# Performance work log

Measured on AMD Instinct MI355X. Metric: run time of the kernel, lower is better.

The kernel has to match this reference:

```python
import jax, jax.numpy as jnp
import numpy as np

B, T, S, I, H = 64, 64, 512, 512, 512

def setup_inputs() -> dict:
    key = jax.random.key(0)
    ks = jax.random.split(key, 9)
    sc = 0.02
    return {
        "input": jax.random.normal(ks[0], (B, T, I), jnp.float32),
        "h0": jax.random.normal(ks[1], (B, H), jnp.float32),
        "c0": jax.random.normal(ks[2], (B, H), jnp.float32),
        "ctx": jax.random.normal(ks[3], (S, B, H), jnp.float32),
        "W_ih": jax.random.normal(ks[4], (4 * H, I), jnp.float32) * sc,
        "b_ih": jax.random.normal(ks[5], (4 * H,), jnp.float32) * sc,
        "W_hh": jax.random.normal(ks[6], (4 * H, H), jnp.float32) * sc,
        "b_hh": jax.random.normal(ks[7], (4 * H,), jnp.float32) * sc,
        "W_out": jax.random.normal(ks[8], (H, 2 * H), jnp.float32) * sc,
    }

def reference(input, h0, c0, ctx, W_ih, b_ih, W_hh, b_hh, W_out):
    ctx_b = ctx.transpose(1, 0, 2)          # (B, S, H)
    x_tm = input.transpose(1, 0, 2)          # (T, B, I) time-major

    def step(carry, x):
        hx, cx = carry
        gates = x @ W_ih.T + b_ih + hx @ W_hh.T + b_hh   # (B, 4H)
        i, f, g, o = jnp.split(gates, 4, axis=1)          # chunk order: in, forget, cell, out
        ct = jax.nn.sigmoid(f) * cx + jax.nn.sigmoid(i) * jnp.tanh(g)
        ht = jax.nn.sigmoid(o) * jnp.tanh(ct)
        # dot attention over source positions
        scores = jnp.einsum('bsh,bh->bs', ctx_b, ht)      # (B, S)
        attn = jax.nn.softmax(scores, axis=1)
        wc = jnp.einsum('bs,bsh->bh', attn, ctx_b)        # (B, H)
        h_tilde = jnp.tanh(jnp.concatenate([wc, ht], axis=1) @ W_out.T)
        return (ht, ct), h_tilde

    (hT, cT), out = jax.lax.scan(step, (h0, c0), x_tm)    # out: (T, B, H)
    return out.transpose(1, 0, 2), hT, cT
```

## Files before the change

### kernel.cpp

```cpp
#include <hip/hip_runtime.h>
#include <hip/hip_bf16.h>

#define NB 64
#define NT_ 64
#define NS 512
#define NI 512
#define NH 512
#define G4 2048
#define H2 1024
#define BT (NB*NT_)
#define RBLK 64
#define CPB 8
#define XWB 512
#define TRB 4096
#define WOB 128
#define GRID_MEGA (RBLK + XWB + TRB + WOB)

typedef __attribute__((ext_vector_type(8))) short short8;
typedef __attribute__((ext_vector_type(4))) float f32x4;

__device__ __forceinline__ short f2bs(float f) {
    __hip_bfloat16 h = __float2bfloat16(f);
    return *reinterpret_cast<short*>(&h);
}
__device__ __forceinline__ float bs2f(short s) {
    unsigned int u = ((unsigned int)(unsigned short)s) << 16;
    union { unsigned int u; float f; } c; c.u = u; return c.f;
}
__device__ __forceinline__ short8 ld8b(const __hip_bfloat16* p) {
    return *reinterpret_cast<const short8*>(p);
}
__device__ __forceinline__ void ld8f2(const float* p, short8& hi, short8& lo) {
    float4 a = *reinterpret_cast<const float4*>(p);
    float4 b = *reinterpret_cast<const float4*>(p + 4);
    float v[8] = {a.x,a.y,a.z,a.w,b.x,b.y,b.z,b.w};
    #pragma unroll
    for (int i = 0; i < 8; i++) {
        short h = f2bs(v[i]);
        hi[i] = h;
        lo[i] = f2bs(v[i] - bs2f(h));
    }
}
__device__ __forceinline__ float fsigm(float x){ return 1.f/(1.f + __expf(-x)); }
__device__ __forceinline__ float ftanh(float x){ float e = __expf(2.f*x); return 1.f - 2.f/(e + 1.f); }

__global__ __launch_bounds__(256) void hseq0_init(const float* __restrict__ h0,
                                                  __hip_bfloat16* __restrict__ hs_h,
                                                  __hip_bfloat16* __restrict__ hs_l,
                                                  unsigned* __restrict__ sync) {
    int i = blockIdx.x*256 + threadIdx.x;
    if (i < 2048) sync[i] = 0u;
    if (i < NB*NH) {
        float x = h0[i];
        __hip_bfloat16 h = __float2bfloat16(x);
        hs_h[i] = h;
        hs_l[i] = __float2bfloat16(x - __bfloat162float(h));
    }
}

__global__ __launch_bounds__(256, 1) void lstm_mega(
    const float* __restrict__ c0,
    const float* __restrict__ W_hh,
    const float* __restrict__ input,
    const float* __restrict__ W_ih,
    const float* __restrict__ b_ih,
    const float* __restrict__ b_hh,
    float* __restrict__ XW2,
    __hip_bfloat16* __restrict__ hs_h,
    __hip_bfloat16* __restrict__ hs_l,
    float* __restrict__ hT, float* __restrict__ cT,
    unsigned* __restrict__ flags,
    unsigned* __restrict__ xwcnt,
    const float* __restrict__ ctx,
    __hip_bfloat16* __restrict__ ctxT,
    const float* __restrict__ W_out,
    __hip_bfloat16* __restrict__ Wout_h,
    __hip_bfloat16* __restrict__ Wout_l)
{
    __shared__ __align__(16) char smem_raw[82432];
    int bid = blockIdx.x;
    int tid = threadIdx.x;
    int lane = tid & 63, w = tid >> 6;
    int fr = lane & 15, fq = lane >> 4;

    if (bid < RBLK) {
        __hip_bfloat16* Wh = (__hip_bfloat16*)smem_raw;
        __hip_bfloat16* Wl = (__hip_bfloat16*)(smem_raw + 32768);
        float (*gl)[32][33] = (float(*)[32][33])(smem_raw + 65536);
        int bi = bid;

        {
            int jl = tid >> 3, ck8 = tid & 7;
            int grow = (jl >> 3) * NH + bi * CPB + (jl & 7);
            const float* src = W_hh + (size_t)grow * NH;
            #pragma unroll
            for (int cc = 0; cc < 8; cc++) {
                int ck = ck8 * 8 + cc;
                short8 hi, lo;
                ld8f2(src + ck*8, hi, lo);
                int sw = (ck * 16) ^ ((jl & 7) << 4);
                *(short8*)((char*)Wh + jl * 1024 + sw) = hi;
                *(short8*)((char*)Wl + jl * 1024 + sw) = lo;
            }
        }
        int eb  = tid >> 2;
        int ec0 = (tid & 3) * 2;
        int ebl = eb & 31, mhalf = eb >> 5;
        float creg[2];
        creg[0] = c0[eb * NH + bi*CPB + ec0];
        creg[1] = c0[eb * NH + bi*CPB + ec0 + 1];
        {
            int guard = 0;
            while (__hip_atomic_load(&xwcnt[0], __ATOMIC_RELAXED, __HIP_MEMORY_SCOPE_AGENT) < 8u) {
                __builtin_amdgcn_s_sleep(1);
                if (++guard > (1<<22)) break;
            }
        }
        float xw[8];
        #pragma unroll
        for (int g = 0; g < 4; g++)
          #pragma unroll
          for (int u = 0; u < 2; u++)
            xw[g*2+u] = XW2[(size_t)eb*G4 + g*NH + bi*CPB + ec0 + u];
        __syncthreads();

        int m0 = (w & 1) * 32;
        int kbase = (w >> 1) * 256;

        for (int t = 0; t < NT_; t++) {
            const __hip_bfloat16* Ah = hs_h + (size_t)t * NB * NH;
            const __hip_bfloat16* Al = hs_l + (size_t)t * NB * NH;

            short8 Aregh[2][8], Aregl[2][8];
            #pragma unroll
            for (int i = 0; i < 2; i++) {
                const __hip_bfloat16* rowH = Ah + (size_t)(m0 + i*16 + fr) * NH + kbase + fq*8;
                const __hip_bfloat16* rowL = Al + (size_t)(m0 + i*16 + fr) * NH + kbase + fq*8;
                #pragma unroll
                for (int k8 = 0; k8 < 8; k8++) {
                    Aregh[i][k8] = ld8b(rowH + k8*32);
                    Aregl[i][k8] = ld8b(rowL + k8*32);
                }
            }

            f32x4 acc[2][2] = {};
            #pragma unroll
            for (int k8 = 0; k8 < 8; k8++) {
                short8 b_h[2], b_l[2];
                #pragma unroll
                for (int j = 0; j < 2; j++) {
                    int jl = j*16 + fr;
                    int byt = jl*1024 + ((((kbase + k8*32 + fq*8)*2)) ^ ((jl & 7) << 4));
                    b_h[j] = *(const short8*)((const char*)Wh + byt);
                    b_l[j] = *(const short8*)((const char*)Wl + byt);
                }
                #pragma unroll
                for (int i = 0; i < 2; i++)
                    #pragma unroll
                    for (int j = 0; j < 2; j++) {
                        acc[i][j] = __builtin_amdgcn_mfma_f32_16x16x32_bf16(Aregh[i][k8], b_h[j], acc[i][j], 0,0,0);
                        acc[i][j] = __builtin_amdgcn_mfma_f32_16x16x32_bf16(Aregh[i][k8], b_l[j], acc[i][j], 0,0,0);
                        acc[i][j] = __builtin_amdgcn_mfma_f32_16x16x32_bf16(Aregl[i][k8], b_h[j], acc[i][j], 0,0,0);
                    }
            }
            #pragma unroll
            for (int i = 0; i < 2; i++)
              #pragma unroll
              for (int j = 0; j < 2; j++)
                #pragma unroll
                for (int r = 0; r < 4; r++)
                    gl[w][i*16 + fq*4 + r][j*16 + fr] = acc[i][j][r];
            __syncthreads();

            float hv[2];
            #pragma unroll
            for (int u = 0; u < 2; u++) {
                int cl = ec0 + u;
                float gi = gl[mhalf][ebl][cl]      + gl[2+mhalf][ebl][cl]      + xw[u];
                float gf = gl[mhalf][ebl][8 + cl]  + gl[2+mhalf][ebl][8 + cl]  + xw[2+u];
                float gg = gl[mhalf][ebl][16 + cl] + gl[2+mhalf][ebl][16 + cl] + xw[4+u];
                float go = gl[mhalf][ebl][24 + cl] + gl[2+mhalf][ebl][24 + cl] + xw[6+u];
                float ct = fsigm(gf)*creg[u] + fsigm(gi)*ftanh(gg);
                hv[u] = fsigm(go)*ftanh(ct);
                creg[u] = ct;
            }
            int hcol = bi*CPB + ec0;
            size_t hoff = (size_t)(t+1)*NB*NH + (size_t)eb*NH + hcol;
            unsigned short h0b = (unsigned short)f2bs(hv[0]);
            unsigned short h1b = (unsigned short)f2bs(hv[1]);
            unsigned ph = (unsigned)h0b | ((unsigned)h1b << 16);
            unsigned short l0b = (unsigned short)f2bs(hv[0] - bs2f((short)h0b));
            unsigned short l1b = (unsigned short)f2bs(hv[1] - bs2f((short)h1b));
            unsigned pl = (unsigned)l0b | ((unsigned)l1b << 16);
            __hip_atomic_store((unsigned*)&hs_h[hoff], ph, __ATOMIC_RELAXED, __HIP_MEMORY_SCOPE_AGENT);
            __hip_atomic_store((unsigned*)&hs_l[hoff], pl, __ATOMIC_RELAXED, __HIP_MEMORY_SCOPE_AGENT);
            if (t == NT_-1) {
                *(float2*)&hT[(size_t)eb*NH + hcol] = make_float2(hv[0], hv[1]);
                *(float2*)&cT[(size_t)eb*NH + hcol] = make_float2(creg[0], creg[1]);
            }

            asm volatile("s_waitcnt vmcnt(0)" ::: "memory");
            __syncthreads();
            if (tid == 0)
                __hip_atomic_store(&flags[bi*16], (unsigned)(t+1), __ATOMIC_RELAXED, __HIP_MEMORY_SCOPE_AGENT);
            if (t + 1 < NT_) {
                int guard = 0;
                while (__hip_atomic_load(&xwcnt[(t+1)*16], __ATOMIC_RELAXED, __HIP_MEMORY_SCOPE_AGENT) < 8u) {
                    __builtin_amdgcn_s_sleep(1);
                    if (++guard > (1<<22)) break;
                }
                #pragma unroll
                for (int g = 0; g < 4; g++)
                  #pragma unroll
                  for (int u = 0; u < 2; u++)
                    xw[g*2+u] = XW2[((size_t)(t+1)*NB + eb)*G4 + g*NH + bi*CPB + ec0 + u];
            }
            {
                unsigned target = (unsigned)(t+1);
                int guard = 0;
                while (__hip_atomic_load(&flags[lane*16], __ATOMIC_RELAXED, __HIP_MEMORY_SCOPE_AGENT) < target) {
                    __builtin_amdgcn_s_sleep(1);
                    if (++guard > (1<<22)) break;
                }
            }
        }
    } else if (bid < RBLK + XWB) {
        int e  = bid - RBLK;
        int t0 = e >> 3;
        int n0 = ((e & 7) * 4 + w) * 64;
        f32x4 acc[4][4] = {};
        for (int kk = 0; kk < NI; kk += 32) {
            short8 ah[4], al[4], bh[4], bl[4];
            #pragma unroll
            for (int i = 0; i < 4; i++)
                ld8f2(input + ((size_t)(i*16+fr)*NT_ + t0)*NI + kk + fq*8, ah[i], al[i]);
            #pragma unroll
            for (int j = 0; j < 4; j++)
                ld8f2(W_ih + (size_t)(n0+j*16+fr)*NI + kk + fq*8, bh[j], bl[j]);
            #pragma unroll
            for (int i = 0; i < 4; i++)
                #pragma unroll
                for (int j = 0; j < 4; j++) {
                    acc[i][j] = __builtin_amdgcn_mfma_f32_16x16x32_bf16(ah[i], bh[j], acc[i][j], 0,0,0);
                    acc[i][j] = __builtin_amdgcn_mfma_f32_16x16x32_bf16(ah[i], bl[j], acc[i][j], 0,0,0);
                    acc[i][j] = __builtin_amdgcn_mfma_f32_16x16x32_bf16(al[i], bh[j], acc[i][j], 0,0,0);
                }
        }
        #pragma unroll
        for (int i = 0; i < 4; i++)
          #pragma unroll
          for (int j = 0; j < 4; j++)
            #pragma unroll
            for (int r = 0; r < 4; r++) {
                int b = i*16 + fq*4 + r;
                int n = n0 + j*16 + fr;
                float v = acc[i][j][r] + b_ih[n] + b_hh[n];
                union { float f; unsigned u; } cv; cv.f = v;
                __hip_atomic_store((unsigned*)&XW2[((size_t)t0*NB + b)*G4 + n], cv.u,
                                   __ATOMIC_RELAXED, __HIP_MEMORY_SCOPE_AGENT);
            }
        asm volatile("s_waitcnt vmcnt(0)" ::: "memory");
        __syncthreads();
        if (tid == 0)
            __hip_atomic_fetch_add(&xwcnt[t0*16], 1u, __ATOMIC_RELAXED, __HIP_MEMORY_SCOPE_AGENT);
    } else if (bid < RBLK + XWB + TRB) {
        float (*tile)[65] = (float(*)[65])smem_raw;
        int tr = bid - (RBLK + XWB);
        int s0 = (tr & 7) * 64, h0 = ((tr >> 3) & 7) * 64, b = tr >> 6;
        int tx = tid & 63, ty = tid >> 6;
        for (int i = 0; i < 16; i++) {
            int s = i*4 + ty;
            tile[s][tx] = ctx[(size_t)(s0+s)*NB*NH + (size_t)b*NH + h0 + tx];
        }
        __syncthreads();
        for (int i = 0; i < 16; i++) {
            int h = i*4 + ty;
            ctxT[(size_t)b*NH*NS + (size_t)(h0+h)*NS + s0 + tx] = __float2bfloat16(tile[tx][h]);
        }
    } else {
        int wv = bid - (RBLK + XWB + TRB);
        for (int i = wv*256 + tid; i < NH*H2; i += WOB*256) {
            float x = W_out[i];
            __hip_bfloat16 h = __float2bfloat16(x);
            Wout_h[i] = h;
            Wout_l[i] = __float2bfloat16(x - __bfloat162float(h));
        }
    }
}

__global__ __launch_bounds__(256) void gemm_scores(const __hip_bfloat16* __restrict__ hs_h,
                                                   const __hip_bfloat16* __restrict__ hs_l,
                                                   const float* __restrict__ ctx,
                                                   float* __restrict__ scores) {
    int wid = blockIdx.x*4 + (threadIdx.x>>6);
    int lane = threadIdx.x & 63;
    int b  = wid >> 3;
    int n0 = (wid & 7) * 64;
    int fr = lane & 15, fq = lane >> 4;
    const __hip_bfloat16* Abh = hs_h + NB*NH + (size_t)b*NH;
    const __hip_bfloat16* Abl = hs_l + NB*NH + (size_t)b*NH;
    const float* Bb = ctx + (size_t)b*NH;
    f32x4 acc[4][4] = {};
    for (int kk = 0; kk < NH; kk += 32) {
        short8 ah[4], al[4], bh[4], bl[4];
        #pragma unroll
        for (int i = 0; i < 4; i++) {
            size_t off = (size_t)(i*16+fr)*NB*NH + kk + fq*8;
            ah[i] = ld8b(Abh + off);
            al[i] = ld8b(Abl + off);
        }
        #pragma unroll
        for (int j = 0; j < 4; j++) ld8f2(Bb + (size_t)(n0+j*16+fr)*NB*NH + kk + fq*8, bh[j], bl[j]);
        #pragma unroll
        for (int i = 0; i < 4; i++)
            #pragma unroll
            for (int j = 0; j < 4; j++) {
                acc[i][j] = __builtin_amdgcn_mfma_f32_16x16x32_bf16(ah[i], bh[j], acc[i][j], 0,0,0);
                acc[i][j] = __builtin_amdgcn_mfma_f32_16x16x32_bf16(ah[i], bl[j], acc[i][j], 0,0,0);
                acc[i][j] = __builtin_amdgcn_mfma_f32_16x16x32_bf16(al[i], bh[j], acc[i][j], 0,0,0);
            }
    }
    #pragma unroll
    for (int i = 0; i < 4; i++)
      #pragma unroll
      for (int j = 0; j < 4; j++)
        #pragma unroll
        for (int r = 0; r < 4; r++) {
            int t = i*16 + fq*4 + r;
            int s = n0 + j*16 + fr;
            scores[((size_t)b*NT_ + t)*NS + s] = acc[i][j][r];
        }
}

__global__ __launch_bounds__(256) void softmax_rows(const float* __restrict__ scores,
                                                    __hip_bfloat16* __restrict__ ah,
                                                    __hip_bfloat16* __restrict__ al) {
    int row = blockIdx.x*4 + (threadIdx.x>>6);
    int lane = threadIdx.x & 63;
    const float* r = scores + (size_t)row*NS;
    float v[8], mx = -1e30f;
    #pragma unroll
    for (int i = 0; i < 8; i++) { v[i] = r[lane + i*64]; mx = fmaxf(mx, v[i]); }
    #pragma unroll
    for (int off = 32; off; off >>= 1) mx = fmaxf(mx, __shfl_xor(mx, off));
    float sum = 0.f;
    #pragma unroll
    for (int i = 0; i < 8; i++) { v[i] = __expf(v[i]-mx); sum += v[i]; }
    #pragma unroll
    for (int off = 32; off; off >>= 1) sum += __shfl_xor(sum, off);
    float inv = 1.f/sum;
    #pragma unroll
    for (int i = 0; i < 8; i++) {
        float a = v[i]*inv;
        __hip_bfloat16 h = __float2bfloat16(a);
        ah[(size_t)row*NS + lane + i*64] = h;
        al[(size_t)row*NS + lane + i*64] = __float2bfloat16(a - __bfloat162float(h));
    }
}

__global__ __launch_bounds__(256) void gemm_wc(const __hip_bfloat16* __restrict__ Ah,
                                               const __hip_bfloat16* __restrict__ Al,
                                               const __hip_bfloat16* __restrict__ ctxT,
                                               float* __restrict__ Wc) {
    int wid = blockIdx.x*4 + (threadIdx.x>>6);
    int lane = threadIdx.x & 63;
    int b  = wid >> 3;
    int n0 = (wid & 7) * 64;
    int fr = lane & 15, fq = lane >> 4;
    const __hip_bfloat16* Abh = Ah + (size_t)b*NT_*NS;
    const __hip_bfloat16* Abl = Al + (size_t)b*NT_*NS;
    const __hip_bfloat16* Bb  = ctxT + (size_t)b*NH*NS;
    f32x4 acc[4][4] = {};
    for (int kk = 0; kk < NS; kk += 32) {
        short8 ah[4], al[4], bb[4];
        #pragma unroll
        for (int i = 0; i < 4; i++) {
            ah[i] = ld8b(Abh + (size_t)(i*16+fr)*NS + kk + fq*8);
            al[i] = ld8b(Abl + (size_t)(i*16+fr)*NS + kk + fq*8);
        }
        #pragma unroll
        for (int j = 0; j < 4; j++) bb[j] = ld8b(Bb + (size_t)(n0+j*16+fr)*NS + kk + fq*8);
        #pragma unroll
        for (int i = 0; i < 4; i++)
            #pragma unroll
            for (int j = 0; j < 4; j++) {
                acc[i][j] = __builtin_amdgcn_mfma_f32_16x16x32_bf16(ah[i], bb[j], acc[i][j], 0,0,0);
                acc[i][j] = __builtin_amdgcn_mfma_f32_16x16x32_bf16(al[i], bb[j], acc[i][j], 0,0,0);
            }
    }
    #pragma unroll
    for (int i = 0; i < 4; i++)
      #pragma unroll
      for (int j = 0; j < 4; j++)
        #pragma unroll
        for (int r = 0; r < 4; r++) {
            int t = i*16 + fq*4 + r;
            int h = n0 + j*16 + fr;
            Wc[((size_t)b*NT_ + t)*NH + h] = acc[i][j][r];
        }
}

__global__ __launch_bounds__(256) void gemm_out(const float* __restrict__ Wc,
                                                const __hip_bfloat16* __restrict__ hs_h,
                                                const __hip_bfloat16* __restrict__ hs_l,
                                                const __hip_bfloat16* __restrict__ Wh,
                                                const __hip_bfloat16* __restrict__ Wl,
                                                float* __restrict__ out) {
    int wid = blockIdx.x*4 + (threadIdx.x>>6);
    int lane = threadIdx.x & 63;
    int m0 = (wid >> 3) * 64;
    int n0 = (wid & 7) * 64;
    int fr = lane & 15, fq = lane >> 4;
    f32x4 acc[4][4] = {};
    for (int kk = 0; kk < NH; kk += 32) {
        short8 ah[4], al[4], bh[4], bl[4];
        #pragma unroll
        for (int i = 0; i < 4; i++) ld8f2(Wc + (size_t)(m0+i*16+fr)*NH + kk + fq*8, ah[i], al[i]);
        #pragma unroll
        for (int j = 0; j < 4; j++) {
            bh[j] = ld8b(Wh + (size_t)(n0+j*16+fr)*H2 + kk + fq*8);
            bl[j] = ld8b(Wl + (size_t)(n0+j*16+fr)*H2 + kk + fq*8);
        }
        #pragma unroll
        for (int i = 0; i < 4; i++)
            #pragma unroll
            for (int j = 0; j < 4; j++) {
                acc[i][j] = __builtin_amdgcn_mfma_f32_16x16x32_bf16(ah[i], bh[j], acc[i][j], 0,0,0);
                acc[i][j] = __builtin_amdgcn_mfma_f32_16x16x32_bf16(ah[i], bl[j], acc[i][j], 0,0,0);
                acc[i][j] = __builtin_amdgcn_mfma_f32_16x16x32_bf16(al[i], bh[j], acc[i][j], 0,0,0);
            }
    }
    {
        const __hip_bfloat16* A2h = hs_h + NB*NH + (size_t)(m0>>6)*NH;
        const __hip_bfloat16* A2l = hs_l + NB*NH + (size_t)(m0>>6)*NH;
        for (int kk = 0; kk < NH; kk += 32) {
            short8 ah[4], al[4], bh[4], bl[4];
            #pragma unroll
            for (int i = 0; i < 4; i++) {
                size_t off = (size_t)(i*16+fr)*NB*NH + kk + fq*8;
                ah[i] = ld8b(A2h + off);
                al[i] = ld8b(A2l + off);
            }
            #pragma unroll
            for (int j = 0; j < 4; j++) {
                bh[j] = ld8b(Wh + (size_t)(n0+j*16+fr)*H2 + NH + kk + fq*8);
                bl[j] = ld8b(Wl + (size_t)(n0+j*16+fr)*H2 + NH + kk + fq*8);
            }
            #pragma unroll
            for (int i = 0; i < 4; i++)
                #pragma unroll
                for (int j = 0; j < 4; j++) {
                    acc[i][j] = __builtin_amdgcn_mfma_f32_16x16x32_bf16(ah[i], bh[j], acc[i][j], 0,0,0);
                    acc[i][j] = __builtin_amdgcn_mfma_f32_16x16x32_bf16(ah[i], bl[j], acc[i][j], 0,0,0);
                    acc[i][j] = __builtin_amdgcn_mfma_f32_16x16x32_bf16(al[i], bh[j], acc[i][j], 0,0,0);
                }
        }
    }
    #pragma unroll
    for (int i = 0; i < 4; i++)
      #pragma unroll
      for (int j = 0; j < 4; j++)
        #pragma unroll
        for (int r = 0; r < 4; r++) {
            int m = m0 + i*16 + fq*4 + r;
            int n = n0 + j*16 + fr;
            out[(size_t)m*NH + n] = ftanh(acc[i][j][r]);
        }
}


extern "C" void kernel_launch(void* const* d_in, const int* in_sizes, int n_in,
                              void* d_out, int out_size, void* d_ws, size_t ws_size,
                              hipStream_t stream) {
    const float* input = (const float*)d_in[0];
    const float* h0    = (const float*)d_in[1];
    const float* c0    = (const float*)d_in[2];
    const float* ctx   = (const float*)d_in[3];
    const float* W_ih  = (const float*)d_in[4];
    const float* b_ih  = (const float*)d_in[5];
    const float* W_hh  = (const float*)d_in[6];
    const float* b_hh  = (const float*)d_in[7];
    const float* W_out = (const float*)d_in[8];
    float* out = (float*)d_out;

    const size_t OFF_XW     = 0;
    const size_t OFF_SCORES = 0;
    const size_t OFF_ATTN_H = 8388608;
    const size_t OFF_ATTN_L = 12582912;
    const size_t OFF_HS_H   = 33554432;
    const size_t OFF_HS_L   = 37814272;
    const size_t OFF_SYNC   = 42074112;
    const size_t OFF_WC     = 42082304;
    const size_t OFF_WOUT_H = 58859520;
    const size_t OFF_WOUT_L = 59908096;
    const size_t OFF_CTXT   = 60956672;
    if (ws_size < 94511104u) return;

    char* ws = (char*)d_ws;
    float*          XW2    = (float*)(ws + OFF_XW);
    float*          scores = (float*)(ws + OFF_SCORES);
    __hip_bfloat16* attn_h = (__hip_bfloat16*)(ws + OFF_ATTN_H);
    __hip_bfloat16* attn_l = (__hip_bfloat16*)(ws + OFF_ATTN_L);
    __hip_bfloat16* hs_h   = (__hip_bfloat16*)(ws + OFF_HS_H);
    __hip_bfloat16* hs_l   = (__hip_bfloat16*)(ws + OFF_HS_L);
    unsigned*       sync   = (unsigned*)(ws + OFF_SYNC);
    unsigned*       flags  = sync;
    unsigned*       xwcnt  = sync + 1024;
    float*          Wc     = (float*)(ws + OFF_WC);
    __hip_bfloat16* Wout_h = (__hip_bfloat16*)(ws + OFF_WOUT_H);
    __hip_bfloat16* Wout_l = (__hip_bfloat16*)(ws + OFF_WOUT_L);
    __hip_bfloat16* ctxT   = (__hip_bfloat16*)(ws + OFF_CTXT);

    hseq0_init<<<128, 256, 0, stream>>>(h0, hs_h, hs_l, sync);

    float* hT = out + (size_t)BT*NH;
    float* cT = hT + NB*NH;
    lstm_mega<<<GRID_MEGA, 256, 0, stream>>>(c0, W_hh, input, W_ih,
                                             b_ih, b_hh, XW2, hs_h, hs_l, hT, cT,
                                             flags, xwcnt, ctx, ctxT, W_out, Wout_h, Wout_l);

    gemm_scores<<<128, 256, 0, stream>>>(hs_h, hs_l, ctx, scores);
    softmax_rows<<<1024, 256, 0, stream>>>(scores, attn_h, attn_l);
    gemm_wc<<<128, 256, 0, stream>>>(attn_h, attn_l, ctxT, Wc);
    gemm_out<<<128, 256, 0, stream>>>(Wc, hs_h, hs_l, Wout_h, Wout_l, out);
}
```

Measured before the change: 627.6 us.

## Fuse attention and output projection into mega kernel, overlapped with recurrence

Removes the four post-recurrence kernels (scores, softmax, weighted context, output GEMM) and adds 128 attention blocks to the persistent mega kernel. Each block handles one batch row and half the timesteps, spin-waiting on recurrence step flags so it can process 16-step chunks while the LSTM is still running. Transpose and W_out conversion blocks now publish completion counters so the attention blocks know when their inputs are ready. This aims to hide attention work behind the serial recurrence and drop the scores, attention and Wc round trips through global memory. In exchange it adds spin-wait polling and co-residency assumptions, and each block reloads ctx and W_out from global memory.

Result: slower. 673.8 us (+7.4%).

```diff
diff --git a/kernel.cpp b/kernel.cpp
--- a/kernel.cpp
+++ b/kernel.cpp
@@ -14,7 +14,8 @@
 #define XWB 512
 #define TRB 4096
 #define WOB 128
-#define GRID_MEGA (RBLK + XWB + TRB + WOB)
+#define ATT 128
+#define GRID_MEGA (RBLK + XWB + TRB + WOB + ATT)
 
 typedef __attribute__((ext_vector_type(8))) short short8;
 typedef __attribute__((ext_vector_type(4))) float f32x4;
@@ -49,7 +50,7 @@
                                                   __hip_bfloat16* __restrict__ hs_l,
                                                   unsigned* __restrict__ sync) {
     int i = blockIdx.x*256 + threadIdx.x;
-    if (i < 2048) sync[i] = 0u;
+    if (i < 4096) sync[i] = 0u;
     if (i < NB*NH) {
         float x = h0[i];
         __hip_bfloat16 h = __float2bfloat16(x);
@@ -71,11 +72,14 @@
     float* __restrict__ hT, float* __restrict__ cT,
     unsigned* __restrict__ flags,
     unsigned* __restrict__ xwcnt,
+    unsigned* __restrict__ trcnt,
+    unsigned* __restrict__ wocnt,
     const float* __restrict__ ctx,
     __hip_bfloat16* __restrict__ ctxT,
     const float* __restrict__ W_out,
     __hip_bfloat16* __restrict__ Wout_h,
-    __hip_bfloat16* __restrict__ Wout_l)
+    __hip_bfloat16* __restrict__ Wout_l,
+    float* __restrict__ out)
 {
     __shared__ __align__(16) char smem_raw[82432];
     int bid = blockIdx.x;
@@ -88,7 +92,6 @@
         __hip_bfloat16* Wl = (__hip_bfloat16*)(smem_raw + 32768);
         float (*gl)[32][33] = (float(*)[32][33])(smem_raw + 65536);
         int bi = bid;
-
         {
             int jl = tid >> 3, ck8 = tid & 7;
             int grow = (jl >> 3) * NH + bi * CPB + (jl & 7);
@@ -130,7 +133,6 @@
         for (int t = 0; t < NT_; t++) {
             const __hip_bfloat16* Ah = hs_h + (size_t)t * NB * NH;
             const __hip_bfloat16* Al = hs_l + (size_t)t * NB * NH;
-
             short8 Aregh[2][8], Aregl[2][8];
             #pragma unroll
             for (int i = 0; i < 2; i++) {
@@ -142,7 +144,6 @@
                     Aregl[i][k8] = ld8b(rowL + k8*32);
                 }
             }
-
             f32x4 acc[2][2] = {};
             #pragma unroll
             for (int k8 = 0; k8 < 8; k8++) {
@@ -198,7 +199,6 @@
                 *(float2*)&hT[(size_t)eb*NH + hcol] = make_float2(hv[0], hv[1]);
                 *(float2*)&cT[(size_t)eb*NH + hcol] = make_float2(creg[0], creg[1]);
             }
-
             asm volatile("s_waitcnt vmcnt(0)" ::: "memory");
             __syncthreads();
             if (tid == 0)
@@ -273,199 +273,183 @@
             tile[s][tx] = ctx[(size_t)(s0+s)*NB*NH + (size_t)b*NH + h0 + tx];
         }
         __syncthreads();
-        for (int i = 0; i < 16; i++) {
-            int h = i*4 + ty;
-            ctxT[(size_t)b*NH*NS + (size_t)(h0+h)*NS + s0 + tx] = __float2bfloat16(tile[tx][h]);
-        }
+        for (int i = 0; i < 8; i++) {
+            int h = i*8 + (tid >> 5);
+            int cp = tid & 31;
+            unsigned short v0 = (unsigned short)f2bs(tile[2*cp][h]);
+            unsigned short v1 = (unsigned short)f2bs(tile[2*cp+1][h]);
+            unsigned pv = (unsigned)v0 | ((unsigned)v1 << 16);
+            __hip_atomic_store((unsigned*)&ctxT[(size_t)b*NH*NS + (size_t)(h0+h)*NS + s0 + 2*cp],
+                               pv, __ATOMIC_RELAXED, __HIP_MEMORY_SCOPE_AGENT);
+        }
+        asm volatile("s_waitcnt vmcnt(0)" ::: "memory");
+        __syncthreads();
+        if (tid == 0)
+            __hip_atomic_fetch_add(&trcnt[b*16], 1u, __ATOMIC_RELAXED, __HIP_MEMORY_SCOPE_AGENT);
+    } else if (bid < RBLK + XWB + TRB + WOB) {
+        int wv = bid - (RBLK + XWB + TRB);
+        for (int p = wv*256 + tid; p < NH*H2/2; p += WOB*256) {
+            float x0 = W_out[2*p], x1 = W_out[2*p+1];
+            unsigned short h0b = (unsigned short)f2bs(x0);
+            unsigned short h1b = (unsigned short)f2bs(x1);
+            unsigned short l0b = (unsigned short)f2bs(x0 - bs2f((short)h0b));
+            unsigned short l1b = (unsigned short)f2bs(x1 - bs2f((short)h1b));
+            __hip_atomic_store((unsigned*)Wout_h + p, (unsigned)h0b | ((unsigned)h1b << 16),
+                               __ATOMIC_RELAXED, __HIP_MEMORY_SCOPE_AGENT);
+            __hip_atomic_store((unsigned*)Wout_l + p, (unsigned)l0b | ((unsigned)l1b << 16),
+                               __ATOMIC_RELAXED, __HIP_MEMORY_SCOPE_AGENT);
+        }
+        asm volatile("s_waitcnt vmcnt(0)" ::: "memory");
+        __syncthreads();
+        if (tid == 0)
+            __hip_atomic_fetch_add(&wocnt[0], 1u, __ATOMIC_RELAXED, __HIP_MEMORY_SCOPE_AGENT);
     } else {
-        int wv = bid - (RBLK + XWB + TRB);
-        for (int i = wv*256 + tid; i < NH*H2; i += WOB*256) {
-            float x = W_out[i];
-            __hip_bfloat16 h = __float2bfloat16(x);
-            Wout_h[i] = h;
-            Wout_l[i] = __float2bfloat16(x - __bfloat162float(h));
+        int at = bid - (RBLK + XWB + TRB + WOB);
+        int b = at >> 1;
+        int halfsel = at & 1;
+        float (*S)[520] = (float(*)[520])smem_raw;
+        __hip_bfloat16 (*WcH)[520] = (__hip_bfloat16(*)[520])smem_raw;
+        __hip_bfloat16 (*WcL)[520] = (__hip_bfloat16(*)[520])(smem_raw + 16640);
+        __hip_bfloat16 (*AtH)[520] = (__hip_bfloat16(*)[520])(smem_raw + 33280);
+        __hip_bfloat16 (*AtL)[520] = (__hip_bfloat16(*)[520])(smem_raw + 49920);
+
+        {
+            int guard = 0;
+            while (__hip_atomic_load(&wocnt[0], __ATOMIC_RELAXED, __HIP_MEMORY_SCOPE_AGENT) < (unsigned)WOB) {
+                __builtin_amdgcn_s_sleep(1);
+                if (++guard > (1<<24)) break;
+            }
+            guard = 0;
+            while (__hip_atomic_load(&trcnt[b*16], __ATOMIC_RELAXED, __HIP_MEMORY_SCOPE_AGENT) < 64u) {
+                __builtin_amdgcn_s_sleep(1);
+                if (++guard > (1<<24)) break;
+            }
+        }
+
+        for (int tg = halfsel*2; tg < halfsel*2 + 2; tg++) {
+            int t0 = tg * 16;
+            {
+                unsigned target = (unsigned)(t0 + 16);
+                int guard = 0;
+                while (__hip_atomic_load(&flags[lane*16], __ATOMIC_RELAXED, __HIP_MEMORY_SCOPE_AGENT) < target) {
+                    __builtin_amdgcn_s_sleep(1);
+                    if (++guard > (1<<24)) break;
+                }
+            }
+
+            {
+                f32x4 sacc[8] = {};
+                const __hip_bfloat16* Ab = hs_h + (size_t)(t0+fr+1)*NB*NH + (size_t)b*NH;
+                const __hip_bfloat16* Al2 = hs_l + (size_t)(t0+fr+1)*NB*NH + (size_t)b*NH;
+                for (int kk = 0; kk < NH; kk += 32) {
+                    short8 ah = ld8b(Ab + kk + fq*8);
+                    short8 al = ld8b(Al2 + kk + fq*8);
+                    #pragma unroll
+                    for (int j = 0; j < 8; j++) {
+                        short8 bh, bl;
+                        ld8f2(ctx + (size_t)(w*128 + j*16 + fr)*NB*NH + (size_t)b*NH + kk + fq*8, bh, bl);
+                        sacc[j] = __builtin_amdgcn_mfma_f32_16x16x32_bf16(ah, bh, sacc[j], 0,0,0);
+                        sacc[j] = __builtin_amdgcn_mfma_f32_16x16x32_bf16(ah, bl, sacc[j], 0,0,0);
+                        sacc[j] = __builtin_amdgcn_mfma_f32_16x16x32_bf16(al, bh, sacc[j], 0,0,0);
+                    }
+                }
+                #pragma unroll
+                for (int j = 0; j < 8; j++)
+                  #pragma unroll
+                  for (int r = 0; r < 4; r++)
+                    S[fq*4 + r][w*128 + j*16 + fr] = sacc[j][r];
+            }
+            __syncthreads();
+
+            for (int rr = 0; rr < 4; rr++) {
+                int row = w*4 + rr;
+                float v[8], mx = -1e30f;
+                #pragma unroll
+                for (int i = 0; i < 8; i++) { v[i] = S[row][lane + i*64]; mx = fmaxf(mx, v[i]); }
+                #pragma unroll
+                for (int off = 32; off; off >>= 1) mx = fmaxf(mx, __shfl_xor(mx, off));
+                float sum = 0.f;
+                #pragma unroll
+                for (int i = 0; i < 8; i++) { v[i] = __expf(v[i]-mx); sum += v[i]; }
+                #pragma unroll
+                for (int off = 32; off; off >>= 1) sum += __shfl_xor(sum, off);
+                float inv = 1.f/sum;
+                #pragma unroll
+                for (int i = 0; i < 8; i++) {
+                    float a = v[i]*inv;
+                    short hb = f2bs(a);
+                    AtH[row][lane + i*64] = *(__hip_bfloat16*)&hb;
+                    short lb = f2bs(a - bs2f(hb));
+                    AtL[row][lane + i*64] = *(__hip_bfloat16*)&lb;
+                }
+            }
+            __syncthreads();
+
+            {
+                f32x4 wacc[8] = {};
+                const __hip_bfloat16* Bb = ctxT + (size_t)b*NH*NS;
+                for (int kk = 0; kk < NS; kk += 32) {
+                    short8 pah = *(const short8*)&AtH[fr][kk + fq*8];
+                    short8 pal = *(const short8*)&AtL[fr][kk + fq*8];
+                    #pragma unroll
+                    for (int j = 0; j < 8; j++) {
+                        short8 cb = ld8b(Bb + (size_t)(w*128 + j*16 + fr)*NS + kk + fq*8);
+                        wacc[j] = __builtin_amdgcn_mfma_f32_16x16x32_bf16(pah, cb, wacc[j], 0,0,0);
+                        wacc[j] = __builtin_amdgcn_mfma_f32_16x16x32_bf16(pal, cb, wacc[j], 0,0,0);
+                    }
+                }
+                #pragma unroll
+                for (int j = 0; j < 8; j++)
+                  #pragma unroll
+                  for (int r = 0; r < 4; r++) {
+                    float v = wacc[j][r];
+                    short hb = f2bs(v);
+                    WcH[fq*4 + r][w*128 + j*16 + fr] = *(__hip_bfloat16*)&hb;
+                    short lb = f2bs(v - bs2f(hb));
+                    WcL[fq*4 + r][w*128 + j*16 + fr] = *(__hip_bfloat16*)&lb;
+                  }
+            }
+            __syncthreads();
+
+            {
+                f32x4 oacc[8] = {};
+                for (int kk = 0; kk < NH; kk += 32) {
+                    short8 ah = *(const short8*)&WcH[fr][kk + fq*8];
+                    short8 al = *(const short8*)&WcL[fr][kk + fq*8];
+                    #pragma unroll
+                    for (int j = 0; j < 8; j++) {
+                        size_t wrow = (size_t)(w*128 + j*16 + fr)*H2 + kk + fq*8;
+                        short8 bh = ld8b(Wout_h + wrow);
+                        short8 bl = ld8b(Wout_l + wrow);
+                        oacc[j] = __builtin_amdgcn_mfma_f32_16x16x32_bf16(ah, bh, oacc[j], 0,0,0);
+                        oacc[j] = __builtin_amdgcn_mfma_f32_16x16x32_bf16(ah, bl, oacc[j], 0,0,0);
+                        oacc[j] = __builtin_amdgcn_mfma_f32_16x16x32_bf16(al, bh, oacc[j], 0,0,0);
+                    }
+                }
+                const __hip_bfloat16* A2h = hs_h + (size_t)(t0+fr+1)*NB*NH + (size_t)b*NH;
+                const __hip_bfloat16* A2l = hs_l + (size_t)(t0+fr+1)*NB*NH + (size_t)b*NH;
+                for (int kk = 0; kk < NH; kk += 32) {
+                    short8 ah = ld8b(A2h + kk + fq*8);
+                    short8 al = ld8b(A2l + kk + fq*8);
+                    #pragma unroll
+                    for (int j = 0; j < 8; j++) {
+                        size_t wrow = (size_t)(w*128 + j*16 + fr)*H2 + NH + kk + fq*8;
+                        short8 bh = ld8b(Wout_h + wrow);
+                        short8 bl = ld8b(Wout_l + wrow);
+                        oacc[j] = __builtin_amdgcn_mfma_f32_16x16x32_bf16(ah, bh, oacc[j], 0,0,0);
+                        oacc[j] = __builtin_amdgcn_mfma_f32_16x16x32_bf16(ah, bl, oacc[j], 0,0,0);
+                        oacc[j] = __builtin_amdgcn_mfma_f32_16x16x32_bf16(al, bh, oacc[j], 0,0,0);
+                    }
+                }
+                #pragma unroll
+                for (int j = 0; j < 8; j++)
+                  #pragma unroll
+                  for (int r = 0; r < 4; r++)
+                    out[(size_t)(b*64 + t0 + fq*4 + r)*NH + w*128 + j*16 + fr] = ftanh(oacc[j][r]);
+            }
+            __syncthreads();
         }
     }
-}
-
-__global__ __launch_bounds__(256) void gemm_scores(const __hip_bfloat16* __restrict__ hs_h,
-                                                   const __hip_bfloat16* __restrict__ hs_l,
-                                                   const float* __restrict__ ctx,
-                                                   float* __restrict__ scores) {
-    int wid = blockIdx.x*4 + (threadIdx.x>>6);
-    int lane = threadIdx.x & 63;
-    int b  = wid >> 3;
-    int n0 = (wid & 7) * 64;
-    int fr = lane & 15, fq = lane >> 4;
-    const __hip_bfloat16* Abh = hs_h + NB*NH + (size_t)b*NH;
-    const __hip_bfloat16* Abl = hs_l + NB*NH + (size_t)b*NH;
-    const float* Bb = ctx + (size_t)b*NH;
-    f32x4 acc[4][4] = {};
-    for (int kk = 0; kk < NH; kk += 32) {
-        short8 ah[4], al[4], bh[4], bl[4];
-        #pragma unroll
-        for (int i = 0; i < 4; i++) {
-            size_t off = (size_t)(i*16+fr)*NB*NH + kk + fq*8;
-            ah[i] = ld8b(Abh + off);
-            al[i] = ld8b(Abl + off);
-        }
-        #pragma unroll
-        for (int j = 0; j < 4; j++) ld8f2(Bb + (size_t)(n0+j*16+fr)*NB*NH + kk + fq*8, bh[j], bl[j]);
-        #pragma unroll
-        for (int i = 0; i < 4; i++)
-            #pragma unroll
-            for (int j = 0; j < 4; j++) {
-                acc[i][j] = __builtin_amdgcn_mfma_f32_16x16x32_bf16(ah[i], bh[j], acc[i][j], 0,0,0);
-                acc[i][j] = __builtin_amdgcn_mfma_f32_16x16x32_bf16(ah[i], bl[j], acc[i][j], 0,0,0);
-                acc[i][j] = __builtin_amdgcn_mfma_f32_16x16x32_bf16(al[i], bh[j], acc[i][j], 0,0,0);
-            }
-    }
-    #pragma unroll
-    for (int i = 0; i < 4; i++)
-      #pragma unroll
-      for (int j = 0; j < 4; j++)
-        #pragma unroll
-        for (int r = 0; r < 4; r++) {
-            int t = i*16 + fq*4 + r;
-            int s = n0 + j*16 + fr;
-            scores[((size_t)b*NT_ + t)*NS + s] = acc[i][j][r];
-        }
-}
-
-__global__ __launch_bounds__(256) void softmax_rows(const float* __restrict__ scores,
-                                                    __hip_bfloat16* __restrict__ ah,
-                                                    __hip_bfloat16* __restrict__ al) {
-    int row = blockIdx.x*4 + (threadIdx.x>>6);
-    int lane = threadIdx.x & 63;
-    const float* r = scores + (size_t)row*NS;
-    float v[8], mx = -1e30f;
-    #pragma unroll
-    for (int i = 0; i < 8; i++) { v[i] = r[lane + i*64]; mx = fmaxf(mx, v[i]); }
-    #pragma unroll
-    for (int off = 32; off; off >>= 1) mx = fmaxf(mx, __shfl_xor(mx, off));
-    float sum = 0.f;
-    #pragma unroll
-    for (int i = 0; i < 8; i++) { v[i] = __expf(v[i]-mx); sum += v[i]; }
-    #pragma unroll
-    for (int off = 32; off; off >>= 1) sum += __shfl_xor(sum, off);
-    float inv = 1.f/sum;
-    #pragma unroll
-    for (int i = 0; i < 8; i++) {
-        float a = v[i]*inv;
-        __hip_bfloat16 h = __float2bfloat16(a);
-        ah[(size_t)row*NS + lane + i*64] = h;
-        al[(size_t)row*NS + lane + i*64] = __float2bfloat16(a - __bfloat162float(h));
-    }
-}
-
-__global__ __launch_bounds__(256) void gemm_wc(const __hip_bfloat16* __restrict__ Ah,
-                                               const __hip_bfloat16* __restrict__ Al,
-                                               const __hip_bfloat16* __restrict__ ctxT,
-                                               float* __restrict__ Wc) {
-    int wid = blockIdx.x*4 + (threadIdx.x>>6);
-    int lane = threadIdx.x & 63;
-    int b  = wid >> 3;
-    int n0 = (wid & 7) * 64;
-    int fr = lane & 15, fq = lane >> 4;
-    const __hip_bfloat16* Abh = Ah + (size_t)b*NT_*NS;
-    const __hip_bfloat16* Abl = Al + (size_t)b*NT_*NS;
-    const __hip_bfloat16* Bb  = ctxT + (size_t)b*NH*NS;
-    f32x4 acc[4][4] = {};
-    for (int kk = 0; kk < NS; kk += 32) {
-        short8 ah[4], al[4], bb[4];
-        #pragma unroll
-        for (int i = 0; i < 4; i++) {
-            ah[i] = ld8b(Abh + (size_t)(i*16+fr)*NS + kk + fq*8);
-            al[i] = ld8b(Abl + (size_t)(i*16+fr)*NS + kk + fq*8);
-        }
-        #pragma unroll
-        for (int j = 0; j < 4; j++) bb[j] = ld8b(Bb + (size_t)(n0+j*16+fr)*NS + kk + fq*8);
-        #pragma unroll
-        for (int i = 0; i < 4; i++)
-            #pragma unroll
-            for (int j = 0; j < 4; j++) {
-                acc[i][j] = __builtin_amdgcn_mfma_f32_16x16x32_bf16(ah[i], bb[j], acc[i][j], 0,0,0);
-                acc[i][j] = __builtin_amdgcn_mfma_f32_16x16x32_bf16(al[i], bb[j], acc[i][j], 0,0,0);
-            }
-    }
-    #pragma unroll
-    for (int i = 0; i < 4; i++)
-      #pragma unroll
-      for (int j = 0; j < 4; j++)
-        #pragma unroll
-        for (int r = 0; r < 4; r++) {
-            int t = i*16 + fq*4 + r;
-            int h = n0 + j*16 + fr;
-            Wc[((size_t)b*NT_ + t)*NH + h] = acc[i][j][r];
-        }
-}
-
-__global__ __launch_bounds__(256) void gemm_out(const float* __restrict__ Wc,
-                                                const __hip_bfloat16* __restrict__ hs_h,
-                                                const __hip_bfloat16* __restrict__ hs_l,
-                                                const __hip_bfloat16* __restrict__ Wh,
-                                                const __hip_bfloat16* __restrict__ Wl,
-                                                float* __restrict__ out) {
-    int wid = blockIdx.x*4 + (threadIdx.x>>6);
-    int lane = threadIdx.x & 63;
-    int m0 = (wid >> 3) * 64;
-    int n0 = (wid & 7) * 64;
-    int fr = lane & 15, fq = lane >> 4;
-    f32x4 acc[4][4] = {};
-    for (int kk = 0; kk < NH; kk += 32) {
-        short8 ah[4], al[4], bh[4], bl[4];
-        #pragma unroll
-        for (int i = 0; i < 4; i++) ld8f2(Wc + (size_t)(m0+i*16+fr)*NH + kk + fq*8, ah[i], al[i]);
-        #pragma unroll
-        for (int j = 0; j < 4; j++) {
-            bh[j] = ld8b(Wh + (size_t)(n0+j*16+fr)*H2 + kk + fq*8);
-            bl[j] = ld8b(Wl + (size_t)(n0+j*16+fr)*H2 + kk + fq*8);
-        }
-        #pragma unroll
-        for (int i = 0; i < 4; i++)
-            #pragma unroll
-            for (int j = 0; j < 4; j++) {
-                acc[i][j] = __builtin_amdgcn_mfma_f32_16x16x32_bf16(ah[i], bh[j], acc[i][j], 0,0,0);
-                acc[i][j] = __builtin_amdgcn_mfma_f32_16x16x32_bf16(ah[i], bl[j], acc[i][j], 0,0,0);
-                acc[i][j] = __builtin_amdgcn_mfma_f32_16x16x32_bf16(al[i], bh[j], acc[i][j], 0,0,0);
-            }
-    }
-    {
-        const __hip_bfloat16* A2h = hs_h + NB*NH + (size_t)(m0>>6)*NH;
-        const __hip_bfloat16* A2l = hs_l + NB*NH + (size_t)(m0>>6)*NH;
-        for (int kk = 0; kk < NH; kk += 32) {
-            short8 ah[4], al[4], bh[4], bl[4];
-            #pragma unroll
-            for (int i = 0; i < 4; i++) {
-                size_t off = (size_t)(i*16+fr)*NB*NH + kk + fq*8;
-                ah[i] = ld8b(A2h + off);
-                al[i] = ld8b(A2l + off);
-            }
-            #pragma unroll
-            for (int j = 0; j < 4; j++) {
-                bh[j] = ld8b(Wh + (size_t)(n0+j*16+fr)*H2 + NH + kk + fq*8);
-                bl[j] = ld8b(Wl + (size_t)(n0+j*16+fr)*H2 + NH + kk + fq*8);
-            }
-            #pragma unroll
-            for (int i = 0; i < 4; i++)
-                #pragma unroll
-                for (int j = 0; j < 4; j++) {
-                    acc[i][j] = __builtin_amdgcn_mfma_f32_16x16x32_bf16(ah[i], bh[j], acc[i][j], 0,0,0);
-                    acc[i][j] = __builtin_amdgcn_mfma_f32_16x16x32_bf16(ah[i], bl[j], acc[i][j], 0,0,0);
-                    acc[i][j] = __builtin_amdgcn_mfma_f32_16x16x32_bf16(al[i], bh[j], acc[i][j], 0,0,0);
-                }
-        }
-    }
-    #pragma unroll
-    for (int i = 0; i < 4; i++)
-      #pragma unroll
-      for (int j = 0; j < 4; j++)
-        #pragma unroll
-        for (int r = 0; r < 4; r++) {
-            int m = m0 + i*16 + fq*4 + r;
-            int n = n0 + j*16 + fr;
-            out[(size_t)m*NH + n] = ftanh(acc[i][j][r]);
-        }
 }
 
 
@@ -484,13 +468,9 @@
     float* out = (float*)d_out;
 
     const size_t OFF_XW     = 0;
-    const size_t OFF_SCORES = 0;
-    const size_t OFF_ATTN_H = 8388608;
-    const size_t OFF_ATTN_L = 12582912;
     const size_t OFF_HS_H   = 33554432;
     const size_t OFF_HS_L   = 37814272;
     const size_t OFF_SYNC   = 42074112;
-    const size_t OFF_WC     = 42082304;
     const size_t OFF_WOUT_H = 58859520;
     const size_t OFF_WOUT_L = 59908096;
     const size_t OFF_CTXT   = 60956672;
@@ -498,15 +478,13 @@
 
     char* ws = (char*)d_ws;
     float*          XW2    = (float*)(ws + OFF_XW);
-    float*          scores = (float*)(ws + OFF_SCORES);
-    __hip_bfloat16* attn_h = (__hip_bfloat16*)(ws + OFF_ATTN_H);
-    __hip_bfloat16* attn_l = (__hip_bfloat16*)(ws + OFF_ATTN_L);
     __hip_bfloat16* hs_h   = (__hip_bfloat16*)(ws + OFF_HS_H);
     __hip_bfloat16* hs_l   = (__hip_bfloat16*)(ws + OFF_HS_L);
     unsigned*       sync   = (unsigned*)(ws + OFF_SYNC);
     unsigned*       flags  = sync;
     unsigned*       xwcnt  = sync + 1024;
-    float*          Wc     = (float*)(ws + OFF_WC);
+    unsigned*       trcnt  = sync + 2048;
+    unsigned*       wocnt  = sync + 3072;
     __hip_bfloat16* Wout_h = (__hip_bfloat16*)(ws + OFF_WOUT_H);
     __hip_bfloat16* Wout_l = (__hip_bfloat16*)(ws + OFF_WOUT_L);
     __hip_bfloat16* ctxT   = (__hip_bfloat16*)(ws + OFF_CTXT);
@@ -517,10 +495,6 @@
     float* cT = hT + NB*NH;
     lstm_mega<<<GRID_MEGA, 256, 0, stream>>>(c0, W_hh, input, W_ih,
                                              b_ih, b_hh, XW2, hs_h, hs_l, hT, cT,
-                                             flags, xwcnt, ctx, ctxT, W_out, Wout_h, Wout_l);
-
-    gemm_scores<<<128, 256, 0, stream>>>(hs_h, hs_l, ctx, scores);
-    softmax_rows<<<1024, 256, 0, stream>>>(scores, attn_h, attn_l);
-    gemm_wc<<<128, 256, 0, stream>>>(attn_h, attn_l, ctxT, Wc);
-    gemm_out<<<128, 256, 0, stream>>>(Wc, hs_h, hs_l, Wout_h, Wout_l, out);
-}
+                                             flags, xwcnt, trcnt, wocnt,
+                                             ctx, ctxT, W_out, Wout_h, Wout_l, out);
+}
```
